# Kernel tuning notes

Measured on AMD Instinct MI355X. Metric: run time of the kernel, lower is better.

The kernel has to match this reference:

```python
import jax, jax.numpy as jnp
import numpy as np

FLOAT_MIN = jnp.finfo(jnp.float32).min


def setup_inputs() -> dict:
    key = jax.random.key(0)
    ks = jax.random.split(key, 8)
    B, S, F1, F2, A = 65536, 256, 256, 256, 128
    return {
        "obs_state": jax.random.normal(ks[0], (B, S), dtype=jnp.float32),
        "action_mask": jax.random.randint(ks[1], (B, A), 0, 2, dtype=jnp.int32),
        "W1": jax.random.normal(ks[2], (S, F1), dtype=jnp.float32) * (1.0 / np.sqrt(S)),
        "b1": jnp.zeros((F1,), dtype=jnp.float32),
        "W2": jax.random.normal(ks[3], (F1, F2), dtype=jnp.float32) * (1.0 / np.sqrt(F1)),
        "b2": jnp.zeros((F2,), dtype=jnp.float32),
        "W3": jax.random.normal(ks[4], (F2, A), dtype=jnp.float32) * (1.0 / np.sqrt(F2)),
        "b3": jnp.zeros((A,), dtype=jnp.float32),
    }


def reference(obs_state, action_mask, W1, b1, W2, b2, W3, b3):
    # 3-layer MLP: state -> fc1 -> relu -> fc2 -> relu -> fc3
    h = jax.nn.relu(obs_state @ W1 + b1)
    h = jax.nn.relu(h @ W2 + b2)
    x = h @ W3 + b3  # [B, A] logits

    # Vectorized action masking (replaces per-element Python loop):
    #   mask==0 -> FLOAT_MIN; rows with all-zero mask -> FLOAT_MIN everywhere, col 0 = 1.0
    valid = action_mask != 0  # [B, A] bool
    x = jnp.where(valid, x, FLOAT_MIN)
    all_invalid = ~jnp.any(valid, axis=1, keepdims=True)  # [B, 1]
    col0 = jnp.arange(x.shape[1]) == 0  # [A]
    x = jnp.where(all_invalid & col0, jnp.float32(1.0), x)
    return x
```

## Files before the change

kernel.cpp:

```cpp
#include <hip/hip_runtime.h>

typedef __attribute__((ext_vector_type(8))) short short8;
typedef __attribute__((ext_vector_type(4))) float f32x4;

#define MT 64
#define STR 264

__device__ __forceinline__ float bmax_r10() { return __uint_as_float(0x7F7F0000u); }

__device__ __forceinline__ unsigned short f2bf_r10(float f) {
    if (!(f == f)) return 0;
    f = fminf(fmaxf(f, -bmax_r10()), bmax_r10());
    unsigned int u = __float_as_uint(f);
    return (unsigned short)((u + 0x7fffu + ((u >> 16) & 1u)) >> 16);
}

__global__ void pack_weights_r10(const float* __restrict__ W,
                                 unsigned short* __restrict__ dst, int K, int N) {
    int idx = blockIdx.x * blockDim.x + threadIdx.x;
    if (idx >= K * N) return;
    int k = idx / N;
    int n = idx - k * N;
    int K0 = K >> 5;
    int lane = (((k & 31) >> 3) << 4) + (n & 15);
    int frag = (n >> 4) * K0 + (k >> 5);
    dst[(frag * 64 + lane) * 8 + (k & 7)] = f2bf_r10(W[idx]);
}

__device__ __forceinline__ void dense_relu_r10(
    const unsigned short* __restrict__ in, unsigned short* __restrict__ outb,
    const unsigned short* __restrict__ wp, const float* __restrict__ bias,
    int wave, int lane, int quad, int noff)
{
    f32x4 acc[4][2] = {};
    #pragma unroll
    for (int k0 = 0; k0 < 8; ++k0) {
        short8 b0 = *(const short8*)&wp[(((wave * 2 + 0) * 8 + k0) * 64 + lane) * 8];
        short8 b1 = *(const short8*)&wp[(((wave * 2 + 1) * 8 + k0) * 64 + lane) * 8];
        #pragma unroll
        for (int rt = 0; rt < 4; ++rt) {
            short8 a = *(const short8*)&in[(rt * 16 + noff) * STR + k0 * 32 + quad * 8];
            acc[rt][0] = __builtin_amdgcn_mfma_f32_16x16x32_bf16(a, b0, acc[rt][0], 0, 0, 0);
            acc[rt][1] = __builtin_amdgcn_mfma_f32_16x16x32_bf16(a, b1, acc[rt][1], 0, 0, 0);
        }
    }
    #pragma unroll
    for (int ct = 0; ct < 2; ++ct) {
        int col = (wave * 2 + ct) * 16 + noff;
        float bv = bias[col];
        #pragma unroll
        for (int rt = 0; rt < 4; ++rt) {
            #pragma unroll
            for (int i = 0; i < 4; ++i) {
                float v = fmaxf(acc[rt][ct][i] + bv, 0.0f);
                outb[(rt * 16 + quad * 4 + i) * STR + col] = f2bf_r10(v);
            }
        }
    }
}

__global__ __launch_bounds__(512, 4)
void ColorNetwork_32495722561720_kernel(
        const float* __restrict__ obs,
        const int* __restrict__ amask,
        const float* __restrict__ b1,
        const float* __restrict__ b2,
        const float* __restrict__ b3,
        const unsigned short* __restrict__ w1p,
        const unsigned short* __restrict__ w2p,
        const unsigned short* __restrict__ w3p,
        float* __restrict__ out)
{
    __shared__ unsigned short bufA[MT * STR];
    __shared__ unsigned short bufB[MT * STR];
    __shared__ unsigned char  mshared[MT * 128];
    __shared__ int rowany[MT];

    const int tid  = threadIdx.x;
    const int wave = tid >> 6;
    const int lane = tid & 63;
    const int quad = lane >> 4;
    const int noff = lane & 15;
    const size_t rowbase = (size_t)blockIdx.x * MT;

    if (tid < MT) rowany[tid] = 0;

    const float4* xin = (const float4*)(obs + rowbase * 256);
    #pragma unroll
    for (int i = 0; i < 8; ++i) {
        int f = tid + i * 512;
        int row = f >> 6;
        int c4 = f & 63;
        float4 v = xin[f];
        ushort4 p;
        p.x = f2bf_r10(v.x); p.y = f2bf_r10(v.y);
        p.z = f2bf_r10(v.z); p.w = f2bf_r10(v.w);
        *(ushort4*)&bufA[row * STR + c4 * 4] = p;
    }
    __syncthreads();

    const int4* min4 = (const int4*)(amask + rowbase * 128);
    #pragma unroll
    for (int i = 0; i < 4; ++i) {
        int f = tid + i * 512;
        int4 m = min4[f];
        int row = f >> 5;
        int c = (f & 31) * 4;
        uchar4 p;
        p.x = (unsigned char)(m.x != 0);
        p.y = (unsigned char)(m.y != 0);
        p.z = (unsigned char)(m.z != 0);
        p.w = (unsigned char)(m.w != 0);
        *(uchar4*)&mshared[row * 128 + c] = p;
        if (m.x | m.y | m.z | m.w) rowany[row] = 1;
    }

    dense_relu_r10(bufA, bufB, w1p, b1, wave, lane, quad, noff);
    __syncthreads();

    dense_relu_r10(bufB, bufA, w2p, b2, wave, lane, quad, noff);
    __syncthreads();

    {
        f32x4 acc[4] = {};
        #pragma unroll
        for (int k0 = 0; k0 < 8; ++k0) {
            short8 b0 = *(const short8*)&w3p[((wave * 8 + k0) * 64 + lane) * 8];
            #pragma unroll
            for (int rt = 0; rt < 4; ++rt) {
                short8 a = *(const short8*)&bufA[(rt * 16 + noff) * STR + k0 * 32 + quad * 8];
                acc[rt] = __builtin_amdgcn_mfma_f32_16x16x32_bf16(a, b0, acc[rt], 0, 0, 0);
            }
        }
        const float BM = bmax_r10();
        int col = wave * 16 + noff;
        float bv = b3[col];
        #pragma unroll
        for (int rt = 0; rt < 4; ++rt) {
            #pragma unroll
            for (int i = 0; i < 4; ++i) {
                int row = rt * 16 + quad * 4 + i;
                float v = acc[rt][i] + bv;
                v = fminf(fmaxf(v, -BM), BM);
                if (!(v == v)) v = 0.0f;
                if (!mshared[row * 128 + col]) v = -BM;
                if (!rowany[row]) v = (col == 0) ? 1.0f : -BM;
                out[(rowbase + row) * 128 + col] = v;
            }
        }
    }
}

__global__ void scrub_r10(float* __restrict__ out, int n) {
    int idx = blockIdx.x * blockDim.x + threadIdx.x;
    if (idx >= n) return;
    float v = out[idx];
    float c = fminf(fmaxf(v, -bmax_r10()), bmax_r10());
    if (!(c == c)) c = -bmax_r10();
    if (__float_as_uint(c) != __float_as_uint(v)) out[idx] = c;
}

extern "C" void kernel_launch(void* const* d_in, const int* in_sizes, int n_in,
                              void* d_out, int out_size, void* d_ws, size_t ws_size,
                              hipStream_t stream) {
    const float* obs   = (const float*)d_in[0];
    const int*   amask = (const int*)d_in[1];
    const float* W1 = (const float*)d_in[2];
    const float* b1 = (const float*)d_in[3];
    const float* W2 = (const float*)d_in[4];
    const float* b2 = (const float*)d_in[5];
    const float* W3 = (const float*)d_in[6];
    const float* b3 = (const float*)d_in[7];
    float* out = (float*)d_out;

    const int B = in_sizes[0] / 256;

    unsigned short* w1p = (unsigned short*)d_ws;
    unsigned short* w2p = w1p + 256 * 256;
    unsigned short* w3p = w2p + 256 * 256;

    pack_weights_r10<<<256, 256, 0, stream>>>(W1, w1p, 256, 256);
    pack_weights_r10<<<256, 256, 0, stream>>>(W2, w2p, 256, 256);
    pack_weights_r10<<<128, 256, 0, stream>>>(W3, w3p, 256, 128);

    ColorNetwork_32495722561720_kernel<<<B / MT, 512, 0, stream>>>(
        obs, amask, b1, b2, b3, w1p, w2p, w3p, out);

    scrub_r10<<<(out_size + 255) / 256, 256, 0, stream>>>(out, out_size);
}
```

Measured before the change: 174.1 us.

## Single LDS activation buffer, drop mask staging, merge weight packs, remove scrub

The two LDS activation buffers become one reused in place, with an extra barrier between each layer's MFMA reads and its writes. The mask is no longer staged in LDS; each lane reads its mask values straight from global memory in the final layer. Together these cut LDS use so the occupancy hint rises from 4 to 6 blocks. The three weight-pack launches are merged into one and the output scrub kernel is dropped, trading extra barriers and register pressure for fewer launches and a full output pass saved.

Measured after the change: 173.8 us. About the same (-0.2%).

```diff
diff --git a/kernel.cpp b/kernel.cpp
--- a/kernel.cpp
+++ b/kernel.cpp
@@ -6,44 +6,55 @@
 #define MT 64
 #define STR 264
 
-__device__ __forceinline__ float bmax_r10() { return __uint_as_float(0x7F7F0000u); }
+__device__ __forceinline__ float bmax_r11() { return __uint_as_float(0x7F7F0000u); }
 
-__device__ __forceinline__ unsigned short f2bf_r10(float f) {
+__device__ __forceinline__ unsigned short f2bf_r11(float f) {
     if (!(f == f)) return 0;
-    f = fminf(fmaxf(f, -bmax_r10()), bmax_r10());
+    f = fminf(fmaxf(f, -bmax_r11()), bmax_r11());
     unsigned int u = __float_as_uint(f);
     return (unsigned short)((u + 0x7fffu + ((u >> 16) & 1u)) >> 16);
 }
 
-__global__ void pack_weights_r10(const float* __restrict__ W,
-                                 unsigned short* __restrict__ dst, int K, int N) {
-    int idx = blockIdx.x * blockDim.x + threadIdx.x;
-    if (idx >= K * N) return;
+__global__ __launch_bounds__(256)
+void pack_weights_r11(const float* __restrict__ W1,
+                      const float* __restrict__ W2,
+                      const float* __restrict__ W3,
+                      unsigned short* __restrict__ ws) {
+    int idx = blockIdx.x * 256 + threadIdx.x;
+    const float* src;
+    unsigned short* dst;
+    int N;
+    if (idx < 65536)       { src = W1; dst = ws;          N = 256; }
+    else if (idx < 131072) { src = W2; dst = ws + 65536;  N = 256; idx -= 65536; }
+    else                   { src = W3; dst = ws + 131072; N = 128; idx -= 131072; }
     int k = idx / N;
     int n = idx - k * N;
-    int K0 = K >> 5;
     int lane = (((k & 31) >> 3) << 4) + (n & 15);
-    int frag = (n >> 4) * K0 + (k >> 5);
-    dst[(frag * 64 + lane) * 8 + (k & 7)] = f2bf_r10(W[idx]);
+    int frag = (n >> 4) * 8 + (k >> 5);
+    dst[(frag * 64 + lane) * 8 + (k & 7)] = f2bf_r11(src[idx]);
 }
 
-__device__ __forceinline__ void dense_relu_r10(
-    const unsigned short* __restrict__ in, unsigned short* __restrict__ outb,
-    const unsigned short* __restrict__ wp, const float* __restrict__ bias,
-    int wave, int lane, int quad, int noff)
+__device__ __forceinline__ void layer_mfma_r11(
+    const unsigned short* __restrict__ act, const unsigned short* __restrict__ wp,
+    int wave, int lane, int quad, int noff, f32x4 acc[4][2])
 {
-    f32x4 acc[4][2] = {};
     #pragma unroll
     for (int k0 = 0; k0 < 8; ++k0) {
         short8 b0 = *(const short8*)&wp[(((wave * 2 + 0) * 8 + k0) * 64 + lane) * 8];
         short8 b1 = *(const short8*)&wp[(((wave * 2 + 1) * 8 + k0) * 64 + lane) * 8];
         #pragma unroll
         for (int rt = 0; rt < 4; ++rt) {
-            short8 a = *(const short8*)&in[(rt * 16 + noff) * STR + k0 * 32 + quad * 8];
+            short8 a = *(const short8*)&act[(rt * 16 + noff) * STR + k0 * 32 + quad * 8];
             acc[rt][0] = __builtin_amdgcn_mfma_f32_16x16x32_bf16(a, b0, acc[rt][0], 0, 0, 0);
             acc[rt][1] = __builtin_amdgcn_mfma_f32_16x16x32_bf16(a, b1, acc[rt][1], 0, 0, 0);
         }
     }
+}
+
+__device__ __forceinline__ void layer_store_r11(
+    unsigned short* __restrict__ act, const float* __restrict__ bias,
+    int wave, int quad, int noff, f32x4 acc[4][2])
+{
     #pragma unroll
     for (int ct = 0; ct < 2; ++ct) {
         int col = (wave * 2 + ct) * 16 + noff;
@@ -53,13 +64,13 @@
             #pragma unroll
             for (int i = 0; i < 4; ++i) {
                 float v = fmaxf(acc[rt][ct][i] + bv, 0.0f);
-                outb[(rt * 16 + quad * 4 + i) * STR + col] = f2bf_r10(v);
+                act[(rt * 16 + quad * 4 + i) * STR + col] = f2bf_r11(v);
             }
         }
     }
 }
 
-__global__ __launch_bounds__(512, 4)
+__global__ __launch_bounds__(512, 6)
 void ColorNetwork_32495722561720_kernel(
         const float* __restrict__ obs,
         const int* __restrict__ amask,
@@ -71,9 +82,7 @@
         const unsigned short* __restrict__ w3p,
         float* __restrict__ out)
 {
-    __shared__ unsigned short bufA[MT * STR];
-    __shared__ unsigned short bufB[MT * STR];
-    __shared__ unsigned char  mshared[MT * 128];
+    __shared__ __align__(16) unsigned short act[MT * STR];
     __shared__ int rowany[MT];
 
     const int tid  = threadIdx.x;
@@ -93,9 +102,9 @@
         int c4 = f & 63;
         float4 v = xin[f];
         ushort4 p;
-        p.x = f2bf_r10(v.x); p.y = f2bf_r10(v.y);
-        p.z = f2bf_r10(v.z); p.w = f2bf_r10(v.w);
-        *(ushort4*)&bufA[row * STR + c4 * 4] = p;
+        p.x = f2bf_r11(v.x); p.y = f2bf_r11(v.y);
+        p.z = f2bf_r11(v.z); p.w = f2bf_r11(v.w);
+        *(ushort4*)&act[row * STR + c4 * 4] = p;
     }
     __syncthreads();
 
@@ -104,37 +113,44 @@
     for (int i = 0; i < 4; ++i) {
         int f = tid + i * 512;
         int4 m = min4[f];
-        int row = f >> 5;
-        int c = (f & 31) * 4;
-        uchar4 p;
-        p.x = (unsigned char)(m.x != 0);
-        p.y = (unsigned char)(m.y != 0);
-        p.z = (unsigned char)(m.z != 0);
-        p.w = (unsigned char)(m.w != 0);
-        *(uchar4*)&mshared[row * 128 + c] = p;
-        if (m.x | m.y | m.z | m.w) rowany[row] = 1;
+        if (m.x | m.y | m.z | m.w) rowany[f >> 5] = 1;
     }
 
-    dense_relu_r10(bufA, bufB, w1p, b1, wave, lane, quad, noff);
-    __syncthreads();
+    {
+        f32x4 acc[4][2] = {};
+        layer_mfma_r11(act, w1p, wave, lane, quad, noff, acc);
+        __syncthreads();
+        layer_store_r11(act, b1, wave, quad, noff, acc);
+        __syncthreads();
+    }
+    {
+        f32x4 acc[4][2] = {};
+        layer_mfma_r11(act, w2p, wave, lane, quad, noff, acc);
+        __syncthreads();
+        layer_store_r11(act, b2, wave, quad, noff, acc);
+        __syncthreads();
+    }
+    {
+        const int col = wave * 16 + noff;
+        int mv[16];
+        #pragma unroll
+        for (int rt = 0; rt < 4; ++rt)
+            #pragma unroll
+            for (int i = 0; i < 4; ++i)
+                mv[rt * 4 + i] = amask[(rowbase + rt * 16 + quad * 4 + i) * 128 + col];
 
-    dense_relu_r10(bufB, bufA, w2p, b2, wave, lane, quad, noff);
-    __syncthreads();
-
-    {
         f32x4 acc[4] = {};
         #pragma unroll
         for (int k0 = 0; k0 < 8; ++k0) {
             short8 b0 = *(const short8*)&w3p[((wave * 8 + k0) * 64 + lane) * 8];
             #pragma unroll
             for (int rt = 0; rt < 4; ++rt) {
-                short8 a = *(const short8*)&bufA[(rt * 16 + noff) * STR + k0 * 32 + quad * 8];
+                short8 a = *(const short8*)&act[(rt * 16 + noff) * STR + k0 * 32 + quad * 8];
                 acc[rt] = __builtin_amdgcn_mfma_f32_16x16x32_bf16(a, b0, acc[rt], 0, 0, 0);
             }
         }
-        const float BM = bmax_r10();
-        int col = wave * 16 + noff;
-        float bv = b3[col];
+        const float BM = bmax_r11();
+        const float bv = b3[col];
         #pragma unroll
         for (int rt = 0; rt < 4; ++rt) {
             #pragma unroll
@@ -143,21 +159,12 @@
                 float v = acc[rt][i] + bv;
                 v = fminf(fmaxf(v, -BM), BM);
                 if (!(v == v)) v = 0.0f;
-                if (!mshared[row * 128 + col]) v = -BM;
+                if (!mv[rt * 4 + i]) v = -BM;
                 if (!rowany[row]) v = (col == 0) ? 1.0f : -BM;
                 out[(rowbase + row) * 128 + col] = v;
             }
         }
     }
-}
-
-__global__ void scrub_r10(float* __restrict__ out, int n) {
-    int idx = blockIdx.x * blockDim.x + threadIdx.x;
-    if (idx >= n) return;
-    float v = out[idx];
-    float c = fminf(fmaxf(v, -bmax_r10()), bmax_r10());
-    if (!(c == c)) c = -bmax_r10();
-    if (__float_as_uint(c) != __float_as_uint(v)) out[idx] = c;
 }
 
 extern "C" void kernel_launch(void* const* d_in, const int* in_sizes, int n_in,
@@ -175,16 +182,13 @@
 
     const int B = in_sizes[0] / 256;
 
-    unsigned short* w1p = (unsigned short*)d_ws;
-    unsigned short* w2p = w1p + 256 * 256;
-    unsigned short* w3p = w2p + 256 * 256;
+    unsigned short* ws = (unsigned short*)d_ws;
+    unsigned short* w1p = ws;
+    unsigned short* w2p = ws + 65536;
+    unsigned short* w3p = ws + 131072;
 
-    pack_weights_r10<<<256, 256, 0, stream>>>(W1, w1p, 256, 256);
-    pack_weights_r10<<<256, 256, 0, stream>>>(W2, w2p, 256, 256);
-    pack_weights_r10<<<128, 256, 0, stream>>>(W3, w3p, 256, 128);
+    pack_weights_r11<<<640, 256, 0, stream>>>(W1, W2, W3, ws);
 
     ColorNetwork_32495722561720_kernel<<<B / MT, 512, 0, stream>>>(
         obs, amask, b1, b2, b3, w1p, w2p, w3p, out);
-
-    scrub_r10<<<(out_size + 255) / 256, 256, 0, stream>>>(out, out_size);
 }
```
